# Optimization experiments

Measured on AMD Instinct MI355X. Metric: run time of the kernel, lower is better.

Reference implementation:

```python
import jax, jax.numpy as jnp
import numpy as np

# Geometry / physics constants (match torch module __init__ kwargs)
NX = 512      # padded grid size
nx = 256      # input speed-map size
nt = 48       # time steps
dt = 0.2
dx = 1.0
nm = 128      # number of measurement sensors on the ring
sr = 8        # transducer subsampling stride -> nr = nm // sr = 16
sR = 200      # ring radius (grid units)
fc = 0.1      # source center frequency
sgma = 2.0    # source gaussian width
t0 = 4.0      # source delay
bg = 1.5      # background speed of sound
ABC_PD = NX // 2 - sR - 1              # 55 : absorbing-layer pad, value 1e-6
PD = (NX - nx) // 2 - ABC_PD           # 73 : background pad, value bg


def setup_inputs() -> dict:
    key = jax.random.key(0)
    # Speed-of-sound map, physical values around bg
    x = bg + 0.1 * jax.random.normal(key, (1, 1, nx, nx), dtype=jnp.float32)
    # Source wavelet: sin(2 pi fc t) * gaussian(t0, sgma)
    times = jnp.arange(nt, dtype=jnp.float32) * dt
    source_intensity = jnp.sin(2 * np.pi * fc * times) * jnp.exp(-(times - t0) ** 2 / (2 * sgma ** 2))
    # Ring sensor indices into flattened NX*NX grid
    thetas = 2 * np.pi * np.arange(nm) / nm
    mx = (NX / 2 + sR * np.cos(thetas)).astype(int)
    my = (NX / 2 + sR * np.sin(thetas)).astype(int)
    meas_inds = jnp.asarray(NX * mx + my, dtype=jnp.int32)   # (nm,)
    trans_inds = meas_inds[::sr]                             # (nr,) = (16,)
    return {"x": x, "source_intensity": source_intensity,
            "meas_inds": meas_inds, "trans_inds": trans_inds}


def _laplacian4(p):
    # 4th-order accurate 5-point stencil along each of the last two axes
    def d2(q, ax):
        return (-jnp.roll(q, 2, ax) + 16 * jnp.roll(q, 1, ax) - 30 * q
                + 16 * jnp.roll(q, -1, ax) - jnp.roll(q, -2, ax)) / 12
    return d2(p, -2) + d2(p, -1)


def reference(x, source_intensity, meas_inds, trans_inds):
    # Pad speed map: interior -> bg, absorbing rim -> 1e-6
    xp = jnp.pad(x, ((0, 0), (0, 0), (PD, PD), (PD, PD)), constant_values=bg)
    xp = jnp.pad(xp, ((0, 0), (0, 0), (ABC_PD, ABC_PD), (ABC_PD, ABC_PD)), constant_values=1e-6)
    B = xp.shape[0]
    N = xp.shape[-1]               # == NX
    nr = trans_inds.shape[0]
    coef = (dt * xp / dx) ** 2     # (B,1,N,N), broadcasts over nr shots
    src_coef = (bg * dt / dx) ** 2
    eye = jnp.eye(nr, dtype=xp.dtype)  # shot i fires only transducer i

    def step(carry, s_j):
        p0, p1 = carry                               # each (B,nr,N,N)
        p = 2 * p1 - p0 + coef * _laplacian4(p1)     # leapfrog update
        pf = p.reshape(B, nr, N * N)
        # Source injection: shot i adds wavelet at trans_inds[i]
        pf = pf.at[:, :, trans_inds].add(src_coef * s_j * eye[None, :, :])
        meas = pf[:, :, meas_inds]                   # (B,nr,nm)
        return (p1, pf.reshape(B, nr, N, N)), meas

    p0 = jnp.zeros((B, nr, N, N), dtype=xp.dtype)
    _, out = jax.lax.scan(step, (p0, p0), source_intensity)  # out: (nt,B,nr,nm)
    return jnp.transpose(out, (1, 2, 3, 0))                  # (B,nr,nm,nt)
```

## Files before the change

kernel.cpp:

```cpp
#include <hip/hip_runtime.h>


typedef unsigned long long u64;
typedef __attribute__((ext_vector_type(4))) unsigned int u32x4;

#define GN     512
#define NMASK  511
#define NCH    16
#define NT     48
#define NM     128
#define WW     208
#define WOFF   103
#define TI     52
#define TS     8
#define NPHASE 6
#define HALO   16
#define LT     84
#define LTS    84
#define LDSE   (LTS*LT)
#define WCELLS (WW*WW)
#define NTH    448
#define NACT   441
#define NBLK   256
#define FQUAD  576
#define FQUAD_A 416
#define NQUAD  1088
#define NQUAD_TB 672
#define NPULLQ 3

__device__ __forceinline__ float4 ld4(const float* p) { return *(const float4*)p; }
__device__ __forceinline__ void st4(float* p, float4 v) { *(float4*)p = v; }
__device__ __forceinline__ float2 ld2(const float* p) { return *(const float2*)p; }

__device__ __forceinline__ unsigned pack2(float c, float p) {
    _Float16 hc = (_Float16)c, hp = (_Float16)p;
    unsigned short uc, up;
    __builtin_memcpy(&uc, &hc, 2); __builtin_memcpy(&up, &hp, 2);
    return (unsigned)uc | ((unsigned)up << 16);
}
__device__ __forceinline__ float2 unpack2(unsigned v) {
    unsigned short uc = (unsigned short)(v & 0xffffu), up = (unsigned short)(v >> 16);
    _Float16 hc, hp;
    __builtin_memcpy(&hc, &uc, 2); __builtin_memcpy(&hp, &up, 2);
    return make_float2((float)hc, (float)hp);
}

__device__ __forceinline__ void st_coh(unsigned* p, u32x4 v) {
    asm volatile("global_store_dwordx4 %0, %1, off sc0 sc1"
                 :: "v"(p), "v"(v) : "memory");
}
__device__ __forceinline__ u32x4 ld_coh(const unsigned* p) {
    u32x4 r;
    asm volatile("global_load_dwordx4 %0, %1, off sc0 sc1"
                 : "=v"(r) : "v"(p) : "memory");
    return r;
}

__device__ __forceinline__ float kcoef(const float* __restrict__ x, int gi, int gj) {
    float xp;
    if (gi < 55 || gi >= 457 || gj < 55 || gj >= 457)
        xp = 1e-6f;
    else if (gi >= 128 && gi < 384 && gj >= 128 && gj < 384)
        xp = x[(gi - 128) * 256 + (gj - 128)];
    else
        xp = 1.5f;
    float t = 0.2f * xp;
    return t * t;
}

__device__ __forceinline__ int tile_sdist(int ti, int tj) {
    int lo = ti * TI - HALO, hi = lo + LT - 1;
    int di = WOFF < lo ? lo - WOFF : (WOFF > hi ? WOFF - hi : 0);
    lo = tj * TI - HALO; hi = lo + LT - 1;
    int dj = WOFF < lo ? lo - WOFF : (WOFF > hi ? WOFF - hi : 0);
    return di > dj ? di : dj;
}
__device__ __forceinline__ bool tile_live(int ti, int tj, int ph) {
    return tile_sdist(ti, tj) <= 2 * (ph * TS + TS) + 4;
}

__global__ __launch_bounds__(NTH, 1)
void persist_kernel(const float* __restrict__ x,
                    const float* __restrict__ src,
                    const int* __restrict__ meas,
                    const int* __restrict__ trans,
                    int* __restrict__ flags,
                    unsigned* __restrict__ GA, unsigned* __restrict__ GB,
                    float* __restrict__ out)
{
    __shared__ float lds0[LDSE];
    __shared__ float lds1[LDSE];
    const int tid  = threadIdx.x;
    const int b    = blockIdx.x;
    const int r    = b & 15;
    const int tile = b >> 4;
    const int tI   = tile >> 2, tJ = tile & 3;
    const int ri0  = tI * TI - HALO;
    const int rj0  = tJ * TI - HALO;

    const bool active = tid < NACT;
    const int ty = tid / 21, tx = tid - 21 * (tid / 21);
    const int li0 = 4 * ty, lj0 = 4 * tx;
    const bool inner = active && tx >= 4 && tx <= 16 && ty >= 4 && ty <= 16;

    for (int q = tid; q < LDSE / 4; q += NTH) {
        st4(&lds0[q * 4], make_float4(0.f, 0.f, 0.f, 0.f));
        st4(&lds1[q * 4], make_float4(0.f, 0.f, 0.f, 0.f));
    }

    const int trv = trans[r];
    const int ox = (trv >> 9) - WOFF, oy = (trv & NMASK) - WOFF;

    float C[16], P[16], K[16];
    #pragma unroll
    for (int i = 0; i < 16; ++i) { C[i] = 0.f; P[i] = 0.f; K[i] = 0.f; }

    int offT2 = 0, offT1 = 0, offB1 = 0, offB2 = 0;
    int offLp[4] = {0,0,0,0}, offRp[4] = {0,0,0,0}, offC[4] = {0,0,0,0};
    unsigned smask = 0;
    if (active) {
        #pragma unroll
        for (int rr = 0; rr < 4; ++rr) {
            int wr = ri0 + li0 + rr;
            #pragma unroll
            for (int cc = 0; cc < 4; ++cc) {
                int wc = rj0 + lj0 + cc;
                K[rr*4+cc] = kcoef(x, (ox + wr) & NMASK, (oy + wc) & NMASK);
            }
        }
        int rT2 = li0 - 2 < 0 ? 0 : li0 - 2;
        int rT1 = li0 - 1 < 0 ? 0 : li0 - 1;
        int rB1 = li0 + 4 > LT - 1 ? LT - 1 : li0 + 4;
        int rB2 = li0 + 5 > LT - 1 ? LT - 1 : li0 + 5;
        offT2 = rT2 * LTS + lj0;  offT1 = rT1 * LTS + lj0;
        offB1 = rB1 * LTS + lj0;  offB2 = rB2 * LTS + lj0;
        #pragma unroll
        for (int rr = 0; rr < 4; ++rr) {
            int base = (li0 + rr) * LTS + lj0;
            offC[rr] = base;
            int ol = base - 2;  if (ol < 0) ol = 0;
            int orr = base + 4; if (orr > LDSE - 2) orr = LDSE - 2;
            offLp[rr] = ol; offRp[rr] = orr;
        }
        int si = (WOFF - ri0) - li0, sj = (WOFF - rj0) - lj0;
        if (si >= 0 && si < 4 && sj >= 0 && sj < 4) smask = 1u << (si * 4 + sj);
    }

    bool mvalid = false; int mlds = 0; float* mout = nullptr;
    if (tid < NM) {
        int mc = meas[tid];
        int mi = ((mc >> 9)    - ox) & NMASK;
        int mj = ((mc & NMASK) - oy) & NMASK;
        int li = mi - ri0, lj = mj - rj0;
        mvalid = (li >= HALO && li < HALO + TI && lj >= HALO && lj < HALO + TI);
        mlds = li * LTS + lj;
        mout = out + (size_t)(r * NM + tid) * NT;
    }

    __syncthreads();

    auto step1 = [&](float (&A)[16], float (&B)[16],
                     const float* rd, float* wb, float sval, int jj) {
        if (active) {
            float t2[4], t1[4], b1a[4], b2a[4];
            float4 v;
            v = ld4(rd + offT2); t2[0]=v.x;  t2[1]=v.y;  t2[2]=v.z;  t2[3]=v.w;
            v = ld4(rd + offT1); t1[0]=v.x;  t1[1]=v.y;  t1[2]=v.z;  t1[3]=v.w;
            v = ld4(rd + offB1); b1a[0]=v.x; b1a[1]=v.y; b1a[2]=v.z; b1a[3]=v.w;
            v = ld4(rd + offB2); b2a[0]=v.x; b2a[1]=v.y; b2a[2]=v.z; b2a[3]=v.w;
            float2 lp[4], rp[4];
            #pragma unroll
            for (int rr = 0; rr < 4; ++rr) {
                lp[rr] = ld2(rd + offLp[rr]);
                rp[rr] = ld2(rd + offRp[rr]);
            }
            #pragma unroll
            for (int rr = 0; rr < 4; ++rr) {
                float h[8];
                h[0]=lp[rr].x; h[1]=lp[rr].y;
                h[2]=B[rr*4+0]; h[3]=B[rr*4+1]; h[4]=B[rr*4+2]; h[5]=B[rr*4+3];
                h[6]=rp[rr].x; h[7]=rp[rr].y;
                #pragma unroll
                for (int cc = 0; cc < 4; ++cc) {
                    float vm2 = (rr == 0) ? t2[cc]  : (rr == 1) ? t1[cc]  : B[(rr-2)*4+cc];
                    float vm1 = (rr == 0) ? t1[cc]  : B[(rr-1)*4+cc];
                    float vp1 = (rr == 3) ? b1a[cc] : B[(rr+1)*4+cc];
                    float vp2 = (rr == 3) ? b2a[cc] : (rr == 2) ? b1a[cc] : B[(rr+2)*4+cc];
                    float c0  = h[cc+2];
                    float lap = (16.f * (h[cc+1] + h[cc+3] + vm1 + vp1)
                                 - (h[cc] + h[cc+4] + vm2 + vp2)
                                 - 60.f * c0) * (1.f / 12.f);
                    float pn = 2.f * c0 - A[rr*4+cc] + K[rr*4+cc] * lap;
                    if (smask & (1u << (rr*4+cc))) pn += sval;
                    A[rr*4+cc] = pn;
                }
                st4(wb + offC[rr],
                    make_float4(A[rr*4+0], A[rr*4+1], A[rr*4+2], A[rr*4+3]));
            }
        }
        __syncthreads();
        if (mvalid) mout[jj] = wb[mlds];
    };

    for (int ph = 0; ph < NPHASE; ++ph) {
        const int J = ph * TS;
        const bool liveSelf = tile_live(tI, tJ, ph);
        unsigned* Wp = ((ph & 1) ? GB : GA) + (size_t)r * WCELLS;
        const bool bnd = ph < NPHASE - 1;
        if (liveSelf) {
            float sv[TS];
            #pragma unroll
            for (int s = 0; s < TS; ++s) sv[s] = 0.09f * src[J + s];
            step1(P, C, lds0, lds1, sv[0], J + 0);
            step1(C, P, lds1, lds0, sv[1], J + 1);
            step1(P, C, lds0, lds1, sv[2], J + 2);
            step1(C, P, lds1, lds0, sv[3], J + 3);
            step1(P, C, lds0, lds1, sv[4], J + 4);
            step1(C, P, lds1, lds0, sv[5], J + 5);
            step1(P, C, lds0, lds1, sv[6], J + 6);
            step1(C, P, lds1, lds0, sv[7], J + 7);
        }
        if (bnd) {
            if (liveSelf) {
                for (int pf = tid; pf < FQUAD; pf += NTH) {
                    int row, col;
                    if (pf < FQUAD_A) {
                        int rA = pf / 13;
                        row = 16 + (rA < 16 ? rA : rA + 20);
                        col = 16 + 4 * (pf - 13 * rA);
                    } else {
                        int p2 = pf - FQUAD_A;
                        int rB = p2 >> 3;
                        int c  = p2 & 7;
                        row = 32 + rB;
                        col = c < 4 ? 16 + 4 * c : 4 * c + 36;
                    }
                    int l = row * LTS + col;
                    u32x4 v;
                    v.x = pack2(lds0[l],     lds1[l]);
                    v.y = pack2(lds0[l + 1], lds1[l + 1]);
                    v.z = pack2(lds0[l + 2], lds1[l + 2]);
                    v.w = pack2(lds0[l + 3], lds1[l + 3]);
                    int gw = (ri0 + row) * WW + (rj0 + col);
                    st_coh(&Wp[gw], v);
                }
                asm volatile("s_waitcnt vmcnt(0)" ::: "memory");
            }
            __syncthreads();
            if (liveSelf && tid == 0)
                __hip_atomic_store(&flags[ph * NBLK + b], 1,
                                   __ATOMIC_RELAXED, __HIP_MEMORY_SCOPE_AGENT);
            const bool liveNext = tile_live(tI, tJ, ph + 1);
            if (liveNext && tid < 9 && tid != 4) {
                int nti = tI + tid / 3 - 1, ntj = tJ + tid % 3 - 1;
                if ((unsigned)nti < 4u && (unsigned)ntj < 4u &&
                    tile_live(nti, ntj, ph)) {
                    int* f = &flags[ph * NBLK + ((((nti << 2) | ntj) << 4) | r)];
                    while (!__hip_atomic_load(f, __ATOMIC_RELAXED,
                                              __HIP_MEMORY_SCOPE_AGENT)) {}
                }
            }
            __syncthreads();
            if (liveNext) {
                u32x4 vv[NPULLQ]; int ll[NPULLQ];
                #pragma unroll
                for (int k = 0; k < NPULLQ; ++k) {
                    vv[k].x = vv[k].y = vv[k].z = vv[k].w = 0u; ll[k] = -1;
                    int p = tid + k * NTH;
                    if (p < NQUAD) {
                        int row, col;
                        if (p < NQUAD_TB) {
                            int rT = p / 21;
                            row = rT < 16 ? rT : rT + 52;
                            col = 4 * (p - 21 * rT);
                        } else {
                            int p2 = p - NQUAD_TB;
                            int rM = p2 >> 3;
                            int c  = p2 & 7;
                            row = 16 + rM;
                            col = c < 4 ? 4 * c : 4 * c + 52;
                        }
                        ll[k] = row * LTS + col;
                        int nti = tI + (row < HALO ? -1 : (row >= HALO + TI ? 1 : 0));
                        int ntj = tJ + (col < HALO ? -1 : (col >= HALO + TI ? 1 : 0));
                        if ((unsigned)nti < 4u && (unsigned)ntj < 4u &&
                            tile_live(nti, ntj, ph)) {
                            int gw = (ri0 + row) * WW + (rj0 + col);
                            vv[k] = ld_coh(&Wp[gw]);
                        } else {
                            ll[k] = -ll[k] - 2;
                        }
                    }
                }
                asm volatile("s_waitcnt vmcnt(0)" ::: "memory");
                #pragma unroll
                for (int k = 0; k < NPULLQ; ++k) {
                    int l = ll[k];
                    bool zf = false;
                    if (l < -1) { l = -l - 2; zf = true; }
                    if (l >= 0) {
                        float4 f0, f1;
                        if (zf) {
                            f0 = make_float4(0.f,0.f,0.f,0.f); f1 = f0;
                        } else {
                            float2 a = unpack2(vv[k].x), bq = unpack2(vv[k].y);
                            float2 c2 = unpack2(vv[k].z), d = unpack2(vv[k].w);
                            f0 = make_float4(a.x, bq.x, c2.x, d.x);
                            f1 = make_float4(a.y, bq.y, c2.y, d.y);
                        }
                        st4(&lds0[l], f0);
                        st4(&lds1[l], f1);
                    }
                }
                __syncthreads();
                if (active && !inner) {
                    #pragma unroll
                    for (int rr = 0; rr < 4; ++rr) {
                        float4 vc = ld4(&lds0[offC[rr]]);
                        float4 vp = ld4(&lds1[offC[rr]]);
                        C[rr*4+0]=vc.x; C[rr*4+1]=vc.y; C[rr*4+2]=vc.z; C[rr*4+3]=vc.w;
                        P[rr*4+0]=vp.x; P[rr*4+1]=vp.y; P[rr*4+2]=vp.z; P[rr*4+3]=vp.w;
                    }
                }
            }
        }
    }
}

extern "C" void kernel_launch(void* const* d_in, const int* in_sizes, int n_in,
                              void* d_out, int out_size, void* d_ws, size_t ws_size,
                              hipStream_t stream)
{
    const float* x     = (const float*)d_in[0];
    const float* src   = (const float*)d_in[1];
    const int*   meas  = (const int*)d_in[2];
    const int*   trans = (const int*)d_in[3];
    float* outp = (float*)d_out;

    int*      flags = (int*)d_ws;
    unsigned* GA = (unsigned*)((char*)d_ws + 8192);
    unsigned* GB = GA + (size_t)NCH * WCELLS;

    hipMemsetAsync(flags, 0, NPHASE * NBLK * sizeof(int), stream);
    hipMemsetAsync(outp, 0, (size_t)out_size * sizeof(float), stream);

    persist_kernel<<<NBLK, NTH, 0, stream>>>(x, src, meas, trans, flags,
                                             GA, GB, outp);
}
```

Before: 71.05 us.

## Split halo exchange per warp with per-direction flags instead of block-wide barriers

```diff
diff --git a/kernel.cpp b/kernel.cpp
--- a/kernel.cpp
+++ b/kernel.cpp
@@ -19,14 +19,9 @@
 #define LTS    84
 #define LDSE   (LTS*LT)
 #define WCELLS (WW*WW)
-#define NTH    448
+#define NTH    512
 #define NACT   441
 #define NBLK   256
-#define FQUAD  576
-#define FQUAD_A 416
-#define NQUAD  1088
-#define NQUAD_TB 672
-#define NPULLQ 3
 
 __device__ __forceinline__ float4 ld4(const float* p) { return *(const float4*)p; }
 __device__ __forceinline__ void st4(float* p, float4 v) { *(float4*)p = v; }
@@ -97,6 +92,8 @@
     const int tI   = tile >> 2, tJ = tile & 3;
     const int ri0  = tI * TI - HALO;
     const int rj0  = tJ * TI - HALO;
+    const int wid  = tid >> 6;
+    const int lane = tid & 63;
 
     const bool active = tid < NACT;
     const int ty = tid / 21, tx = tid - 21 * (tid / 21);
@@ -221,106 +218,96 @@
             step1(C, P, lds1, lds0, sv[7], J + 7);
         }
         if (bnd) {
-            if (liveSelf) {
-                for (int pf = tid; pf < FQUAD; pf += NTH) {
-                    int row, col;
-                    if (pf < FQUAD_A) {
-                        int rA = pf / 13;
-                        row = 16 + (rA < 16 ? rA : rA + 20);
-                        col = 16 + 4 * (pf - 13 * rA);
-                    } else {
-                        int p2 = pf - FQUAD_A;
-                        int rB = p2 >> 3;
-                        int c  = p2 & 7;
-                        row = 32 + rB;
-                        col = c < 4 ? 16 + 4 * c : 4 * c + 36;
+            const bool liveNext = tile_live(tI, tJ, ph + 1);
+            if (liveSelf && wid < 4) {
+                #pragma unroll
+                for (int k = 0; k < 4; ++k) {
+                    int q = lane + 64 * k;
+                    if (q < 208) {
+                        int row, col;
+                        if (wid == 0)      { int qr = q / 13; row = 16 + qr; col = 16 + 4 * (q - 13 * qr); }
+                        else if (wid == 1) { int qr = q / 13; row = 52 + qr; col = 16 + 4 * (q - 13 * qr); }
+                        else if (wid == 2) { row = 16 + (q >> 2); col = 16 + 4 * (q & 3); }
+                        else               { row = 16 + (q >> 2); col = 52 + 4 * (q & 3); }
+                        int l = row * LTS + col;
+                        u32x4 v;
+                        v.x = pack2(lds0[l],     lds1[l]);
+                        v.y = pack2(lds0[l + 1], lds1[l + 1]);
+                        v.z = pack2(lds0[l + 2], lds1[l + 2]);
+                        v.w = pack2(lds0[l + 3], lds1[l + 3]);
+                        st_coh(&Wp[(ri0 + row) * WW + (rj0 + col)], v);
                     }
-                    int l = row * LTS + col;
-                    u32x4 v;
-                    v.x = pack2(lds0[l],     lds1[l]);
-                    v.y = pack2(lds0[l + 1], lds1[l + 1]);
-                    v.z = pack2(lds0[l + 2], lds1[l + 2]);
-                    v.w = pack2(lds0[l + 3], lds1[l + 3]);
-                    int gw = (ri0 + row) * WW + (rj0 + col);
-                    st_coh(&Wp[gw], v);
                 }
                 asm volatile("s_waitcnt vmcnt(0)" ::: "memory");
-            }
-            __syncthreads();
-            if (liveSelf && tid == 0)
-                __hip_atomic_store(&flags[ph * NBLK + b], 1,
-                                   __ATOMIC_RELAXED, __HIP_MEMORY_SCOPE_AGENT);
-            const bool liveNext = tile_live(tI, tJ, ph + 1);
-            if (liveNext && tid < 9 && tid != 4) {
-                int nti = tI + tid / 3 - 1, ntj = tJ + tid % 3 - 1;
-                if ((unsigned)nti < 4u && (unsigned)ntj < 4u &&
-                    tile_live(nti, ntj, ph)) {
-                    int* f = &flags[ph * NBLK + ((((nti << 2) | ntj) << 4) | r)];
+                if (lane == 0)
+                    __hip_atomic_store(&flags[(ph * NBLK + b) * 4 + wid], 1,
+                                       __ATOMIC_RELAXED, __HIP_MEMORY_SCOPE_AGENT);
+            }
+            if (liveNext) {
+                int dti, dtj, fb;
+                if      (wid == 0) { dti = -1; dtj =  0; fb = 1; }
+                else if (wid == 1) { dti =  1; dtj =  0; fb = 0; }
+                else if (wid == 2) { dti =  0; dtj = -1; fb = 3; }
+                else if (wid == 3) { dti =  0; dtj =  1; fb = 2; }
+                else if (wid == 4) { dti = -1; dtj = -1; fb = 1; }
+                else if (wid == 5) { dti = -1; dtj =  1; fb = 1; }
+                else if (wid == 6) { dti =  1; dtj = -1; fb = 0; }
+                else               { dti =  1; dtj =  1; fb = 0; }
+                int nti = tI + dti, ntj = tJ + dtj;
+                const bool has = ((unsigned)nti < 4u) && ((unsigned)ntj < 4u) &&
+                                 tile_live(nti, ntj, ph);
+                if (has) {
+                    int* f = &flags[(ph * NBLK + ((((nti << 2) | ntj) << 4) | r)) * 4 + fb];
                     while (!__hip_atomic_load(f, __ATOMIC_RELAXED,
                                               __HIP_MEMORY_SCOPE_AGENT)) {}
                 }
-            }
-            __syncthreads();
-            if (liveNext) {
-                u32x4 vv[NPULLQ]; int ll[NPULLQ];
-                #pragma unroll
-                for (int k = 0; k < NPULLQ; ++k) {
+                const int NQ = (wid < 4) ? 208 : 64;
+                u32x4 vv[4]; int ll[4];
+                #pragma unroll
+                for (int k = 0; k < 4; ++k) {
                     vv[k].x = vv[k].y = vv[k].z = vv[k].w = 0u; ll[k] = -1;
-                    int p = tid + k * NTH;
-                    if (p < NQUAD) {
+                    int q = lane + 64 * k;
+                    if (q < NQ) {
                         int row, col;
-                        if (p < NQUAD_TB) {
-                            int rT = p / 21;
-                            row = rT < 16 ? rT : rT + 52;
-                            col = 4 * (p - 21 * rT);
-                        } else {
-                            int p2 = p - NQUAD_TB;
-                            int rM = p2 >> 3;
-                            int c  = p2 & 7;
-                            row = 16 + rM;
-                            col = c < 4 ? 4 * c : 4 * c + 52;
-                        }
+                        if      (wid == 0) { int qr = q / 13; row = qr;            col = 16 + 4 * (q - 13 * qr); }
+                        else if (wid == 1) { int qr = q / 13; row = 68 + qr;       col = 16 + 4 * (q - 13 * qr); }
+                        else if (wid == 2) { row = 16 + (q >> 2); col = 4 * (q & 3); }
+                        else if (wid == 3) { row = 16 + (q >> 2); col = 68 + 4 * (q & 3); }
+                        else if (wid == 4) { row = (q >> 2);      col = 4 * (q & 3); }
+                        else if (wid == 5) { row = (q >> 2);      col = 68 + 4 * (q & 3); }
+                        else if (wid == 6) { row = 68 + (q >> 2); col = 4 * (q & 3); }
+                        else               { row = 68 + (q >> 2); col = 68 + 4 * (q & 3); }
                         ll[k] = row * LTS + col;
-                        int nti = tI + (row < HALO ? -1 : (row >= HALO + TI ? 1 : 0));
-                        int ntj = tJ + (col < HALO ? -1 : (col >= HALO + TI ? 1 : 0));
-                        if ((unsigned)nti < 4u && (unsigned)ntj < 4u &&
-                            tile_live(nti, ntj, ph)) {
-                            int gw = (ri0 + row) * WW + (rj0 + col);
-                            vv[k] = ld_coh(&Wp[gw]);
-                        } else {
-                            ll[k] = -ll[k] - 2;
-                        }
+                        if (has)
+                            vv[k] = ld_coh(&Wp[(ri0 + row) * WW + (rj0 + col)]);
                     }
                 }
-                asm volatile("s_waitcnt vmcnt(0)" ::: "memory");
-                #pragma unroll
-                for (int k = 0; k < NPULLQ; ++k) {
-                    int l = ll[k];
-                    bool zf = false;
-                    if (l < -1) { l = -l - 2; zf = true; }
-                    if (l >= 0) {
+                if (has) asm volatile("s_waitcnt vmcnt(0)" ::: "memory");
+                #pragma unroll
+                for (int k = 0; k < 4; ++k) {
+                    if (ll[k] >= 0) {
                         float4 f0, f1;
-                        if (zf) {
-                            f0 = make_float4(0.f,0.f,0.f,0.f); f1 = f0;
-                        } else {
+                        if (has) {
                             float2 a = unpack2(vv[k].x), bq = unpack2(vv[k].y);
                             float2 c2 = unpack2(vv[k].z), d = unpack2(vv[k].w);
                             f0 = make_float4(a.x, bq.x, c2.x, d.x);
                             f1 = make_float4(a.y, bq.y, c2.y, d.y);
+                        } else {
+                            f0 = make_float4(0.f, 0.f, 0.f, 0.f); f1 = f0;
                         }
-                        st4(&lds0[l], f0);
-                        st4(&lds1[l], f1);
+                        st4(&lds0[ll[k]], f0);
+                        st4(&lds1[ll[k]], f1);
                     }
                 }
-                __syncthreads();
-                if (active && !inner) {
-                    #pragma unroll
-                    for (int rr = 0; rr < 4; ++rr) {
-                        float4 vc = ld4(&lds0[offC[rr]]);
-                        float4 vp = ld4(&lds1[offC[rr]]);
-                        C[rr*4+0]=vc.x; C[rr*4+1]=vc.y; C[rr*4+2]=vc.z; C[rr*4+3]=vc.w;
-                        P[rr*4+0]=vp.x; P[rr*4+1]=vp.y; P[rr*4+2]=vp.z; P[rr*4+3]=vp.w;
-                    }
+            }
+            __syncthreads();
+            if (liveNext && active && !inner) {
+                #pragma unroll
+                for (int rr = 0; rr < 4; ++rr) {
+                    float4 vc = ld4(&lds0[offC[rr]]);
+                    float4 vp = ld4(&lds1[offC[rr]]);
+                    C[rr*4+0]=vc.x; C[rr*4+1]=vc.y; C[rr*4+2]=vc.z; C[rr*4+3]=vc.w;
+                    P[rr*4+0]=vp.x; P[rr*4+1]=vp.y; P[rr*4+2]=vp.z; P[rr*4+3]=vp.w;
                 }
             }
         }
@@ -338,10 +325,10 @@
     float* outp = (float*)d_out;
 
     int*      flags = (int*)d_ws;
-    unsigned* GA = (unsigned*)((char*)d_ws + 8192);
+    unsigned* GA = (unsigned*)((char*)d_ws + 32768);
     unsigned* GB = GA + (size_t)NCH * WCELLS;
 
-    hipMemsetAsync(flags, 0, NPHASE * NBLK * sizeof(int), stream);
+    hipMemsetAsync(flags, 0, (NPHASE - 1) * NBLK * 4 * sizeof(int), stream);
     hipMemsetAsync(outp, 0, (size_t)out_size * sizeof(float), stream);
 
     persist_kernel<<<NBLK, NTH, 0, stream>>>(x, src, meas, trans, flags,
```

New measurement: 72.96 us. 2.7% more time.
